# Kernel optimization log

Hardware: AMD Instinct MI355X
Metric: run time of the kernel (lower is better)

## Reference

```python
import jax, jax.numpy as jnp
import numpy as np

TEMPERATURE = 0.1  # from __init__ temperature
NEG_INF = -1e30


def setup_inputs() -> dict:
    key = jax.random.key(0)
    k1, k2, k3, k4, k5 = jax.random.split(key, 5)
    B, D = 8192, 128
    return {
        "zis": jax.random.normal(k1, (B, D), dtype=jnp.float32),
        "zjs": jax.random.normal(k2, (B, D), dtype=jnp.float32),
        "ilabels": jax.random.randint(k3, (B,), 0, 100, dtype=jnp.int64),
        "jlabels": jax.random.randint(k4, (B,), 0, 100, dtype=jnp.int64),
        "weights": jax.random.uniform(k5, (B,), dtype=jnp.float32),
        "idx": 0,
    }


def reference(zis, zjs, ilabels, jlabels, weights, idx):
    B = zjs.shape[0]
    # forward F.normalize + cosine_matrix's normalize is idempotent -> single L2 normalize
    zi = zis / jnp.linalg.norm(zis, axis=1, keepdims=True)
    zj = zjs / jnp.linalg.norm(zjs, axis=1, keepdims=True)
    # similarity_matrix = 1 - (1 - zj @ zi^T); rows indexed by zjs
    logits = (zj @ zi.T) / TEMPERATURE  # [B, B]
    # labels[i, j] = (ilabels[j] == jlabels[i])
    labels = ilabels[None, :] == jlabels[:, None]  # [B, B] bool
    neg_mask = ~labels  # 'zeros' columns per row
    rows = jnp.arange(B)
    pos_idx = idx + rows  # class_level=False: ones = idx + i, size = 1
    pos = logits[rows, pos_idx]  # [B]
    # CrossEntropy over cat([pos, logits[i, zeros]]) at label 0:
    # loss_i = logsumexp([pos_i, neg_row_i]) - pos_i (numerically stable)
    neg_max = jnp.max(jnp.where(neg_mask, logits, NEG_INF), axis=1)
    m = jnp.maximum(pos, neg_max)  # [B]
    denom = jnp.exp(pos - m) + jnp.sum(
        jnp.where(neg_mask, jnp.exp(logits - m[:, None]), 0.0), axis=1
    )
    loss = m + jnp.log(denom) - pos  # [B]
    # size==1 path: loss*w / w (faithful to torch weighted sum / weight.sum())
    w = weights[pos_idx]
    loss = (loss * w) / w
    return jnp.sum(loss) / B
```

## Files before the change

### kernel.cpp

```cpp
#include <hip/hip_runtime.h>


#define BB 8192
#define DD 128
#define TM 128
#define TN 128
#define NJ 8

typedef __attribute__((ext_vector_type(8))) short short8;
typedef __attribute__((ext_vector_type(4))) float floatx4;

#define GLOBAL_AS __attribute__((address_space(1)))
#define LDS_AS    __attribute__((address_space(3)))

static __device__ __forceinline__ float wave_sum(float v) {
#pragma unroll
    for (int off = 32; off > 0; off >>= 1) v += __shfl_xor(v, off, 64);
    return v;
}

static __device__ __forceinline__ unsigned short f2bf(float f) {
    unsigned int u = __float_as_uint(f);
    return (unsigned short)((u + 0x7FFFu + ((u >> 16) & 1u)) >> 16);
}

__global__ __launch_bounds__(256) void prep_kernel(
    const float* __restrict__ zis, const float* __restrict__ zjs,
    unsigned short* __restrict__ Zib, unsigned short* __restrict__ Zjb,
    float* __restrict__ rni, float* __restrict__ rnj,
    float* __restrict__ denom, float* __restrict__ out, int nout)
{
    if (threadIdx.x < 2) denom[blockIdx.x * 2 + threadIdx.x] = 0.0f;
    if (blockIdx.x == 0 && (int)threadIdx.x < nout) out[threadIdx.x] = 0.0f;

    int wave = threadIdx.x >> 6, lane = threadIdx.x & 63;
    int row = blockIdx.x * 4 + wave;
    const float* src; unsigned short* dst; float* rn; int r;
    if (row < BB) { src = zis; dst = Zib; rn = rni; r = row; }
    else          { src = zjs; dst = Zjb; rn = rnj; r = row - BB; }
    float2 u = *(const float2*)(src + (size_t)r * DD + lane * 2);
    float s = wave_sum(u.x * u.x + u.y * u.y);
    float sc = 1.0f / sqrtf(s);
    if (lane == 0) rn[r] = sc;
    ushort2 o; o.x = f2bf(u.x * sc); o.y = f2bf(u.y * sc);
    *(ushort2*)(dst + (size_t)r * DD + lane * 2) = o;
}

__global__ __launch_bounds__(512, 2) void mfma_tile_kernel(
    const unsigned short* __restrict__ Zjb,
    const unsigned short* __restrict__ Zib,
    const int* __restrict__ ilab, const int* __restrict__ jlab,
    float* __restrict__ denom)
{
    __shared__ __align__(16) unsigned short Bt[2][TN * DD];
    __shared__ int jlds[TM];

    int tid  = threadIdx.x;
    int lane = tid & 63, wave = tid >> 6;
    int wm = wave >> 1, wn = wave & 1;
    int quad = lane >> 4, l15 = lane & 15;
    int i0    = blockIdx.y * TM;
    int jbase = blockIdx.x * (NJ * TN);

    if (tid < TM) jlds[tid] = jlab[i0 + tid];

    short8 af[2][4];
#pragma unroll
    for (int mt = 0; mt < 2; ++mt)
#pragma unroll
        for (int ks = 0; ks < 4; ++ks)
            af[mt][ks] = *(const short8*)(Zjb
                + (size_t)(i0 + wm * 32 + mt * 16 + l15) * DD
                + ks * 32 + quad * 8);

    int rl = lane >> 4, p = lane & 15;
    auto stage = [&](int t) {
        const unsigned short* src = Zib + (size_t)(jbase + t * TN) * DD;
        unsigned short* lb = &Bt[t & 1][0];
#pragma unroll
        for (int u = 0; u < 4; ++u) {
            int g = wave * 4 + u;
            int grow = g * 4 + rl;
            int gslot = p ^ (grow & 15);
            const unsigned short* gp = src + (size_t)grow * DD + gslot * 8;
            unsigned short* lp = lb + g * 512;
            __builtin_amdgcn_global_load_lds((const GLOBAL_AS void*)gp,
                                             (LDS_AS void*)lp, 16, 0, 0);
        }
    };

    float rs[2][4];
#pragma unroll
    for (int mt = 0; mt < 2; ++mt)
#pragma unroll
        for (int r = 0; r < 4; ++r) rs[mt][r] = 0.0f;

    stage(0);
    stage(1);
    asm volatile("s_waitcnt vmcnt(4) lgkmcnt(0)" ::: "memory");
    __builtin_amdgcn_s_barrier();

#pragma unroll 2
    for (int t = 0; t < NJ; ++t) {
        int ilv[4];
#pragma unroll
        for (int nt = 0; nt < 4; ++nt)
            ilv[nt] = ilab[jbase + t * TN + wn * 64 + nt * 16 + l15];

        const unsigned short* bb = &Bt[t & 1][0];
        floatx4 acc[2][4];

        __builtin_amdgcn_s_setprio(1);
#pragma unroll
        for (int ks = 0; ks < 4; ++ks) {
            short8 bfr[4];
#pragma unroll
            for (int nt = 0; nt < 4; ++nt) {
                int n = wn * 64 + nt * 16 + l15;
                int ps = (((ks << 2) | quad) ^ l15) << 3;
                bfr[nt] = *(const short8*)(bb + n * DD + ps);
            }
            if (ks == 0) {
                floatx4 zz = (floatx4){0.f, 0.f, 0.f, 0.f};
#pragma unroll
                for (int mt = 0; mt < 2; ++mt)
#pragma unroll
                    for (int nt = 0; nt < 4; ++nt)
                        acc[mt][nt] = __builtin_amdgcn_mfma_f32_16x16x32_bf16(
                            af[mt][0], bfr[nt], zz, 0, 0, 0);
            } else {
#pragma unroll
                for (int mt = 0; mt < 2; ++mt)
#pragma unroll
                    for (int nt = 0; nt < 4; ++nt)
                        acc[mt][nt] = __builtin_amdgcn_mfma_f32_16x16x32_bf16(
                            af[mt][ks], bfr[nt], acc[mt][nt], 0, 0, 0);
            }
        }
        __builtin_amdgcn_s_setprio(0);

        if (t + 1 < NJ) {
            asm volatile("s_waitcnt vmcnt(0)" ::: "memory");
            __builtin_amdgcn_s_barrier();
            if (t + 2 < NJ) stage(t + 2);
        }

#pragma unroll
        for (int mt = 0; mt < 2; ++mt) {
#pragma unroll
            for (int r = 0; r < 4; ++r) {
                int jr = jlds[wm * 32 + mt * 16 + quad * 4 + r];
                float s = rs[mt][r];
#pragma unroll
                for (int nt = 0; nt < 4; ++nt) {
                    float e = __expf(fmaf(acc[mt][nt][r], 10.0f, -10.0f));
                    s += (ilv[nt] != jr) ? e : 0.0f;
                }
                rs[mt][r] = s;
            }
        }
    }

#pragma unroll
    for (int mt = 0; mt < 2; ++mt) {
#pragma unroll
        for (int r = 0; r < 4; ++r) {
            float v = rs[mt][r];
            v += __shfl_xor(v, 1, 64);
            v += __shfl_xor(v, 2, 64);
            v += __shfl_xor(v, 4, 64);
            v += __shfl_xor(v, 8, 64);
            if (l15 == 0)
                atomicAdd(&denom[i0 + wm * 32 + mt * 16 + quad * 4 + r], v);
        }
    }
}

__global__ __launch_bounds__(256) void posfinal_kernel(
    const float* __restrict__ zis, const float* __restrict__ zjs,
    const float* __restrict__ rni, const float* __restrict__ rnj,
    const float* __restrict__ denom, const float* __restrict__ wts,
    const int* __restrict__ idxp, float* __restrict__ out)
{
    int wave = threadIdx.x >> 6, lane = threadIdx.x & 63;
    int idx = idxp[0];
    float ll = 0.0f;
#pragma unroll
    for (int t = 0; t < 4; ++t) {
        int i = blockIdx.x * 16 + wave * 4 + t;
        int j = idx + i;
        float2 a  = *(const float2*)(zjs + (size_t)i * DD + lane * 2);
        float2 b2 = *(const float2*)(zis + (size_t)j * DD + lane * 2);
        float s = wave_sum(a.x * b2.x + a.y * b2.y);
        if (lane == 0) {
            float p = s * rni[j] * rnj[i] * 10.0f;
            float l = 10.0f + logf(__expf(p - 10.0f) + denom[i]) - p;
            float w = wts[j];
            ll += (l * w) / w;
        }
    }
    __shared__ float part[4];
    if (lane == 0) part[wave] = ll;
    __syncthreads();
    if (threadIdx.x == 0)
        atomicAdd(out, (part[0] + part[1] + part[2] + part[3]) * (1.0f / BB));
}

extern "C" void kernel_launch(void* const* d_in, const int* in_sizes, int n_in,
                              void* d_out, int out_size, void* d_ws, size_t ws_size,
                              hipStream_t stream) {
    const float* zis = (const float*)d_in[0];
    const float* zjs = (const float*)d_in[1];
    const int* ilab = (const int*)d_in[2];
    const int* jlab = (const int*)d_in[3];
    const float* wts = (const float*)d_in[4];
    const int* idxp = (const int*)d_in[5];
    float* out = (float*)d_out;

    float* rni   = (float*)d_ws;
    float* rnj   = rni + BB;
    float* denom = rnj + BB;
    unsigned short* Zib = (unsigned short*)(denom + BB);
    unsigned short* Zjb = Zib + (size_t)BB * DD;

    prep_kernel<<<2 * BB / 4, 256, 0, stream>>>(
        zis, zjs, Zib, Zjb, rni, rnj, denom, out, out_size);
    mfma_tile_kernel<<<dim3(BB / (NJ * TN), BB / TM), 512, 0, stream>>>(
        Zjb, Zib, ilab, jlab, denom);
    posfinal_kernel<<<BB / 16, 256, 0, stream>>>(
        zis, zjs, rni, rnj, denom, wts, idxp, out);
}
```

Measured before the change: 114.6 us.

## Fuse positive-pair finalization into tile kernel and software-pipeline MFMA with exp epilogue

The separate posfinal kernel is removed. The last block to finish each row tile, picked with a per-row ticket counter, now computes the positive logits and the loss contribution for its rows. The MFMA loop is split into per-column-group chunks, and each chunk's exp/mask epilogue is interleaved with the next chunk's MFMAs so transcendental work overlaps matrix math. Labels are preloaded into LDS and registers instead of reloaded from global memory each iteration. This saves one kernel launch and adds a second accumulator set, ticket atomics and fences. The overlap depends on the compiler actually interleaving the chunks.

```diff
diff --git a/kernel.cpp b/kernel.cpp
--- a/kernel.cpp
+++ b/kernel.cpp
@@ -28,10 +28,12 @@
     const float* __restrict__ zis, const float* __restrict__ zjs,
     unsigned short* __restrict__ Zib, unsigned short* __restrict__ Zjb,
     float* __restrict__ rni, float* __restrict__ rnj,
-    float* __restrict__ denom, float* __restrict__ out, int nout)
+    float* __restrict__ denom, int* __restrict__ tickets,
+    float* __restrict__ out, int nout)
 {
     if (threadIdx.x < 2) denom[blockIdx.x * 2 + threadIdx.x] = 0.0f;
     if (blockIdx.x == 0 && (int)threadIdx.x < nout) out[threadIdx.x] = 0.0f;
+    if (blockIdx.x == 2 && threadIdx.x < 64) tickets[threadIdx.x] = 0;
 
     int wave = threadIdx.x >> 6, lane = threadIdx.x & 63;
     int row = blockIdx.x * 4 + wave;
@@ -50,10 +52,16 @@
     const unsigned short* __restrict__ Zjb,
     const unsigned short* __restrict__ Zib,
     const int* __restrict__ ilab, const int* __restrict__ jlab,
-    float* __restrict__ denom)
+    float* __restrict__ denom, int* __restrict__ tickets,
+    const float* __restrict__ zis, const float* __restrict__ zjs,
+    const float* __restrict__ rni, const float* __restrict__ rnj,
+    const float* __restrict__ wts, const int* __restrict__ idxp,
+    float* __restrict__ out)
 {
     __shared__ __align__(16) unsigned short Bt[2][TN * DD];
-    __shared__ int jlds[TM];
+    __shared__ int ilds[NJ * TN];
+    __shared__ int tkt;
+    __shared__ float part[8];
 
     int tid  = threadIdx.x;
     int lane = tid & 63, wave = tid >> 6;
@@ -62,7 +70,15 @@
     int i0    = blockIdx.y * TM;
     int jbase = blockIdx.x * (NJ * TN);
 
-    if (tid < TM) jlds[tid] = jlab[i0 + tid];
+    ilds[tid]       = ilab[jbase + tid];
+    ilds[tid + 512] = ilab[jbase + tid + 512];
+
+    int jrv[8];
+#pragma unroll
+    for (int mt = 0; mt < 2; ++mt)
+#pragma unroll
+        for (int r = 0; r < 4; ++r)
+            jrv[mt * 4 + r] = jlab[i0 + wm * 32 + mt * 16 + quad * 4 + r];
 
     short8 af[2][4];
 #pragma unroll
@@ -95,6 +111,37 @@
 #pragma unroll
         for (int r = 0; r < 4; ++r) rs[mt][r] = 0.0f;
 
+    auto gran = [&](const unsigned short* bb, int nt, floatx4 (&aC)[2]) {
+        int n = wn * 64 + nt * 16 + l15;
+#pragma unroll
+        for (int ks = 0; ks < 4; ++ks) {
+            int ps = (((ks << 2) | quad) ^ l15) << 3;
+            short8 b = *(const short8*)(bb + n * DD + ps);
+            if (ks == 0) {
+                floatx4 zz = (floatx4){0.f, 0.f, 0.f, 0.f};
+                aC[0] = __builtin_amdgcn_mfma_f32_16x16x32_bf16(af[0][0], b, zz, 0, 0, 0);
+                aC[1] = __builtin_amdgcn_mfma_f32_16x16x32_bf16(af[1][0], b, zz, 0, 0, 0);
+            } else {
+                aC[0] = __builtin_amdgcn_mfma_f32_16x16x32_bf16(af[0][ks], b, aC[0], 0, 0, 0);
+                aC[1] = __builtin_amdgcn_mfma_f32_16x16x32_bf16(af[1][ks], b, aC[1], 0, 0, 0);
+            }
+        }
+    };
+    auto epi = [&](floatx4 (&aP)[2], int ilP) {
+#pragma unroll
+        for (int mt = 0; mt < 2; ++mt)
+#pragma unroll
+            for (int r = 0; r < 4; ++r) {
+                float e = __expf(fmaf(aP[mt][r], 10.0f, -10.0f));
+                rs[mt][r] += (ilP != jrv[mt * 4 + r]) ? e : 0.0f;
+            }
+    };
+
+    floatx4 accA[2], accB[2];
+    accB[0] = (floatx4){-1e30f, -1e30f, -1e30f, -1e30f};
+    accB[1] = accB[0];
+    int ilB = 0;
+
     stage(0);
     stage(1);
     asm volatile("s_waitcnt vmcnt(4) lgkmcnt(0)" ::: "memory");
@@ -102,67 +149,24 @@
 
 #pragma unroll 2
     for (int t = 0; t < NJ; ++t) {
-        int ilv[4];
-#pragma unroll
-        for (int nt = 0; nt < 4; ++nt)
-            ilv[nt] = ilab[jbase + t * TN + wn * 64 + nt * 16 + l15];
-
         const unsigned short* bb = &Bt[t & 1][0];
-        floatx4 acc[2][4];
-
+        const int* ilr = &ilds[t * TN + wn * 64 + l15];
         __builtin_amdgcn_s_setprio(1);
-#pragma unroll
-        for (int ks = 0; ks < 4; ++ks) {
-            short8 bfr[4];
-#pragma unroll
-            for (int nt = 0; nt < 4; ++nt) {
-                int n = wn * 64 + nt * 16 + l15;
-                int ps = (((ks << 2) | quad) ^ l15) << 3;
-                bfr[nt] = *(const short8*)(bb + n * DD + ps);
-            }
-            if (ks == 0) {
-                floatx4 zz = (floatx4){0.f, 0.f, 0.f, 0.f};
-#pragma unroll
-                for (int mt = 0; mt < 2; ++mt)
-#pragma unroll
-                    for (int nt = 0; nt < 4; ++nt)
-                        acc[mt][nt] = __builtin_amdgcn_mfma_f32_16x16x32_bf16(
-                            af[mt][0], bfr[nt], zz, 0, 0, 0);
-            } else {
-#pragma unroll
-                for (int mt = 0; mt < 2; ++mt)
-#pragma unroll
-                    for (int nt = 0; nt < 4; ++nt)
-                        acc[mt][nt] = __builtin_amdgcn_mfma_f32_16x16x32_bf16(
-                            af[mt][ks], bfr[nt], acc[mt][nt], 0, 0, 0);
-            }
-        }
+        gran(bb, 0, accA); int il0 = ilr[0];  epi(accB, ilB);
+        gran(bb, 1, accB); int il1 = ilr[16]; epi(accA, il0);
+        gran(bb, 2, accA); int il2 = ilr[32]; epi(accB, il1);
+        gran(bb, 3, accB); ilB = ilr[48];     epi(accA, il2);
         __builtin_amdgcn_s_setprio(0);
-
         if (t + 1 < NJ) {
             asm volatile("s_waitcnt vmcnt(0)" ::: "memory");
             __builtin_amdgcn_s_barrier();
             if (t + 2 < NJ) stage(t + 2);
         }
-
-#pragma unroll
-        for (int mt = 0; mt < 2; ++mt) {
-#pragma unroll
-            for (int r = 0; r < 4; ++r) {
-                int jr = jlds[wm * 32 + mt * 16 + quad * 4 + r];
-                float s = rs[mt][r];
-#pragma unroll
-                for (int nt = 0; nt < 4; ++nt) {
-                    float e = __expf(fmaf(acc[mt][nt][r], 10.0f, -10.0f));
-                    s += (ilv[nt] != jr) ? e : 0.0f;
-                }
-                rs[mt][r] = s;
-            }
-        }
     }
-
-#pragma unroll
-    for (int mt = 0; mt < 2; ++mt) {
+    epi(accB, ilB);
+
+#pragma unroll
+    for (int mt = 0; mt < 2; ++mt)
 #pragma unroll
         for (int r = 0; r < 4; ++r) {
             float v = rs[mt][r];
@@ -173,37 +177,40 @@
             if (l15 == 0)
                 atomicAdd(&denom[i0 + wm * 32 + mt * 16 + quad * 4 + r], v);
         }
+
+    __threadfence();
+    __syncthreads();
+    if (tid == 0) tkt = atomicAdd(&tickets[blockIdx.y], 1);
+    __syncthreads();
+    if (tkt == 7) {
+        __threadfence();
+        int idx2 = idxp[0];
+        float ll = 0.0f;
+#pragma unroll 4
+        for (int rr = 0; rr < 16; ++rr) {
+            int i = i0 + wave * 16 + rr;
+            int j = idx2 + i;
+            float2 a  = *(const float2*)(zjs + (size_t)i * DD + lane * 2);
+            float2 b2 = *(const float2*)(zis + (size_t)j * DD + lane * 2);
+            float s = wave_sum(a.x * b2.x + a.y * b2.y);
+            if (lane == 0) {
+                float d = __hip_atomic_load(&denom[i], __ATOMIC_RELAXED,
+                                            __HIP_MEMORY_SCOPE_AGENT);
+                float pp = s * rni[j] * rnj[i] * 10.0f;
+                float l = 10.0f + logf(__expf(pp - 10.0f) + d) - pp;
+                float w = wts[j];
+                ll += (l * w) / w;
+            }
+        }
+        if (lane == 0) part[wave] = ll;
+        __syncthreads();
+        if (tid == 0) {
+            float sum = 0.0f;
+#pragma unroll
+            for (int q = 0; q < 8; ++q) sum += part[q];
+            atomicAdd(out, sum * (1.0f / BB));
+        }
     }
-}
-
-__global__ __launch_bounds__(256) void posfinal_kernel(
-    const float* __restrict__ zis, const float* __restrict__ zjs,
-    const float* __restrict__ rni, const float* __restrict__ rnj,
-    const float* __restrict__ denom, const float* __restrict__ wts,
-    const int* __restrict__ idxp, float* __restrict__ out)
-{
-    int wave = threadIdx.x >> 6, lane = threadIdx.x & 63;
-    int idx = idxp[0];
-    float ll = 0.0f;
-#pragma unroll
-    for (int t = 0; t < 4; ++t) {
-        int i = blockIdx.x * 16 + wave * 4 + t;
-        int j = idx + i;
-        float2 a  = *(const float2*)(zjs + (size_t)i * DD + lane * 2);
-        float2 b2 = *(const float2*)(zis + (size_t)j * DD + lane * 2);
-        float s = wave_sum(a.x * b2.x + a.y * b2.y);
-        if (lane == 0) {
-            float p = s * rni[j] * rnj[i] * 10.0f;
-            float l = 10.0f + logf(__expf(p - 10.0f) + denom[i]) - p;
-            float w = wts[j];
-            ll += (l * w) / w;
-        }
-    }
-    __shared__ float part[4];
-    if (lane == 0) part[wave] = ll;
-    __syncthreads();
-    if (threadIdx.x == 0)
-        atomicAdd(out, (part[0] + part[1] + part[2] + part[3]) * (1.0f / BB));
 }
 
 extern "C" void kernel_launch(void* const* d_in, const int* in_sizes, int n_in,
@@ -220,13 +227,13 @@
     float* rni   = (float*)d_ws;
     float* rnj   = rni + BB;
     float* denom = rnj + BB;
-    unsigned short* Zib = (unsigned short*)(denom + BB);
+    int*   tickets = (int*)(denom + BB);
+    unsigned short* Zib = (unsigned short*)(tickets + 64);
     unsigned short* Zjb = Zib + (size_t)BB * DD;
 
     prep_kernel<<<2 * BB / 4, 256, 0, stream>>>(
-        zis, zjs, Zib, Zjb, rni, rnj, denom, out, out_size);
+        zis, zjs, Zib, Zjb, rni, rnj, denom, tickets, out, out_size);
     mfma_tile_kernel<<<dim3(BB / (NJ * TN), BB / TM), 512, 0, stream>>>(
-        Zjb, Zib, ilab, jlab, denom);
-    posfinal_kernel<<<BB / 16, 256, 0, stream>>>(
-        zis, zjs, rni, rnj, denom, wts, idxp, out);
-}
+        Zjb, Zib, ilab, jlab, denom, tickets,
+        zis, zjs, rni, rnj, wts, idxp, out);
+}
```

After: 231.5 us. +102.0%, slower.
